# Optimization experiments

Measured on AMD Instinct MI355X. Metric: run time of the kernel, lower is better.

The kernel has to match this reference:

```python
import jax, jax.numpy as jnp
import numpy as np

B, S, D, H, M = 4, 1024, 1024, 16, 128
HD = D // H  # 64


def setup_inputs() -> dict:
    key = jax.random.key(0)
    ks = jax.random.split(key, 12)
    s = 0.02
    return {
        "x": jax.random.normal(ks[0], (B, S, D), dtype=jnp.float32),
        "Wq": jax.random.normal(ks[1], (D, D), dtype=jnp.float32) * s,
        "bq": jnp.zeros((D,), dtype=jnp.float32),
        "Wk": jax.random.normal(ks[2], (D, D), dtype=jnp.float32) * s,
        "bk": jnp.zeros((D,), dtype=jnp.float32),
        "Wv": jax.random.normal(ks[3], (D, D), dtype=jnp.float32) * s,
        "bv": jnp.zeros((D,), dtype=jnp.float32),
        "Wo": jax.random.normal(ks[4], (D, D), dtype=jnp.float32) * s,
        "bo": jnp.zeros((D,), dtype=jnp.float32),
        "u": jax.random.normal(ks[5], (H, HD), dtype=jnp.float32) * s,
        "v": jax.random.normal(ks[6], (H, HD), dtype=jnp.float32) * s,
    }


def _rel_sinusoid_emb():
    # [2M+1, HD] sinusoidal embeddings over relative offsets -M..M
    rel_range = jnp.arange(-M, M + 1, dtype=jnp.float32)
    inv_freq = 1.0 / (10000.0 ** (jnp.arange(0, HD, 2, dtype=jnp.float32) / HD))
    sinusoid = rel_range[:, None] * inv_freq[None, :]  # [2M+1, HD/2]
    emb = jnp.zeros((2 * M + 1, HD), dtype=jnp.float32)
    emb = emb.at[:, 0::2].set(jnp.sin(sinusoid))
    emb = emb.at[:, 1::2].set(jnp.cos(sinusoid))
    return emb


def reference(x, Wq, bq, Wk, bk, Wv, bv, Wo, bo, u, v):
    scale = 1.0 / np.sqrt(HD).astype(np.float32)

    def heads(t):  # [B,S,D] -> [B,H,S,HD]
        return t.reshape(B, S, H, HD).transpose(0, 2, 1, 3)

    q = heads(x @ Wq + bq)
    k = heads(x @ Wk + bk)
    vv = heads(x @ Wv + bv)

    rel_emb = _rel_sinusoid_emb()  # [2M+1, HD]
    pos = jnp.arange(S)
    rel_index = jnp.clip(pos[None, :] - pos[:, None], -M, M) + M  # [S,S] int

    q_u = q + u[None, :, None, :]
    q_v = q + v[None, :, None, :]

    content = jnp.einsum("bhid,bhjd->bhij", q_u, k) * scale  # [B,H,S,S]
    # einsum('bhid,ijd->bhij', q_v, rel_emb[rel_index]) == gather of per-bucket scores
    rel_all = jnp.einsum("bhid,rd->bhir", q_v, rel_emb) * scale  # [B,H,S,2M+1]
    rel_scores = jnp.take_along_axis(rel_all, rel_index[None, None, :, :], axis=-1)

    attn = jax.nn.softmax(content + rel_scores, axis=-1)
    out = jnp.einsum("bhij,bhjd->bhid", attn, vv)  # [B,H,S,HD]
    out = out.transpose(0, 2, 1, 3).reshape(B, S, D)
    return out @ Wo + bo
```

## Files before the change

### kernel.cpp

```cpp
#include <hip/hip_runtime.h>
#include <math.h>


#define BB 4
#define SS 1024
#define DD 1024
#define HH 16
#define HDIM 64
#define SCALE 0.125f
#define KMAX_BOUND 16.0f

typedef __attribute__((ext_vector_type(8))) short short8;
typedef __attribute__((ext_vector_type(4))) float f32x4;
typedef __attribute__((ext_vector_type(4))) unsigned short us4;
typedef unsigned short u16;

#define MFMA __builtin_amdgcn_mfma_f32_16x16x32_bf16

__device__ __forceinline__ float b2f(u16 v) {
  return __uint_as_float((unsigned)v << 16);
}
__device__ __forceinline__ u16 f2b(float f) {
  unsigned u = __float_as_uint(f);
  return (u16)((u + 0x7FFF + ((u >> 16) & 1)) >> 16);
}
__device__ __forceinline__ void gl_lds16(const u16* g, u16* l) {
  __builtin_amdgcn_global_load_lds(
      (const __attribute__((address_space(1))) unsigned int*)(g),
      (__attribute__((address_space(3))) unsigned int*)(l), 16, 0, 0);
}

__global__ __launch_bounds__(256) void prep(
    const float* __restrict__ x,
    const float* __restrict__ W0, const float* __restrict__ W1,
    const float* __restrict__ W2, const float* __restrict__ W3,
    u16* __restrict__ xb,
    u16* __restrict__ T0, u16* __restrict__ T1,
    u16* __restrict__ T2, u16* __restrict__ T3,
    u16* __restrict__ Eb) {
  __shared__ float t[64 * 68];
  const int bid = blockIdx.x, tid = threadIdx.x;
  if (bid < 2048) {
    const size_t i = ((size_t)bid * 256 + tid) * 8;
    float4 a = *reinterpret_cast<const float4*>(&x[i]);
    float4 b = *reinterpret_cast<const float4*>(&x[i + 4]);
    short8 v;
    v[0] = (short)f2b(a.x); v[1] = (short)f2b(a.y);
    v[2] = (short)f2b(a.z); v[3] = (short)f2b(a.w);
    v[4] = (short)f2b(b.x); v[5] = (short)f2b(b.y);
    v[6] = (short)f2b(b.z); v[7] = (short)f2b(b.w);
    *reinterpret_cast<short8*>(&xb[i]) = v;
  } else if (bid < 3072) {
    const int wz = bid - 2048;
    const int z = wz >> 8;
    const float* W = z == 0 ? W0 : z == 1 ? W1 : z == 2 ? W2 : W3;
    u16* T = z == 0 ? T0 : z == 1 ? T1 : z == 2 ? T2 : T3;
    const int k0 = ((wz >> 4) & 15) * 64, n0 = (wz & 15) * 64;
#pragma unroll
    for (int rd = 0; rd < 4; ++rd) {
      const int idx = rd * 256 + tid;
      const int r = idx >> 4, c4 = (idx & 15) * 4;
      *reinterpret_cast<float4*>(&t[r * 68 + c4]) =
          *reinterpret_cast<const float4*>(&W[(size_t)(k0 + r) * DD + n0 + c4]);
    }
    __syncthreads();
#pragma unroll
    for (int rd = 0; rd < 2; ++rd) {
      const int idx = rd * 256 + tid;
      const int rr = idx >> 3, cc = (idx & 7) * 8;
      short8 v;
#pragma unroll
      for (int e = 0; e < 8; ++e) v[e] = (short)f2b(t[(cc + e) * 68 + rr]);
      *reinterpret_cast<short8*>(&T[(size_t)(n0 + rr) * DD + k0 + cc]) = v;
    }
  } else {
    const int j = (bid - 3072) * 4 + (tid >> 6);
    const int d = tid & 63;
    const int pair = d >> 1;
    const float inv_freq =
        exp2f(-((float)(2 * pair) / 64.0f) * 13.287712379549449f);
    const float arg = (float)j * inv_freq;
    const float val = (d & 1) ? cosf(arg) : sinf(arg);
    Eb[j * 64 + d] = f2b(val);
  }
}

__global__ __launch_bounds__(256, 3) void gemm_mfma(
    const u16* __restrict__ A,
    const u16* __restrict__ W0, const u16* __restrict__ W1, const u16* __restrict__ W2,
    const float* __restrict__ b0, const float* __restrict__ b1, const float* __restrict__ b2,
    void* o0, void* o1, void* o2, int final_mode) {
  const int z = blockIdx.z;
  const u16* Bt = z == 0 ? W0 : z == 1 ? W1 : W2;
  const float* bias = z == 0 ? b0 : z == 1 ? b1 : b2;
  __shared__ u16 As0[128 * 32];
  __shared__ u16 Bs0[128 * 32];
  __shared__ u16 As1[128 * 32];
  __shared__ u16 Bs1[128 * 32];
  const int tid = threadIdx.x;
  const int bm = blockIdx.y * 128, bn = blockIdx.x * 128;
  const int lane = tid & 63, w = tid >> 6;
  const int wr = w >> 1, wc = w & 1;
  const int lr = lane & 15, lg = lane >> 4;

  const int r_i0 = 32 * w + (lane >> 2);
  const int r_i1 = r_i0 + 16;
  const int q0 = (lane & 3) ^ ((r_i0 >> 1) & 3);
  const int q1 = (lane & 3) ^ ((r_i1 >> 1) & 3);
  const u16* gA0 = &A[(size_t)(bm + r_i0) * DD + q0 * 8];
  const u16* gA1 = &A[(size_t)(bm + r_i1) * DD + q1 * 8];
  const u16* gB0 = &Bt[(size_t)(bn + r_i0) * DD + q0 * 8];
  const u16* gB1 = &Bt[(size_t)(bn + r_i1) * DD + q1 * 8];
  const int lo0 = (32 * w) * 32;
  const int lo1 = (32 * w + 16) * 32;

  const f32x4 Z4 = {0.f, 0.f, 0.f, 0.f};
  f32x4 acc[4][4];
#pragma unroll
  for (int m = 0; m < 4; ++m)
#pragma unroll
    for (int n = 0; n < 4; ++n) acc[m][n] = Z4;

  auto STAGE = [&](u16* Ab, u16* Bb, int kk) {
    gl_lds16(gA0 + kk, Ab + lo0);
    gl_lds16(gA1 + kk, Ab + lo1);
    gl_lds16(gB0 + kk, Bb + lo0);
    gl_lds16(gB1 + kk, Bb + lo1);
  };
  auto COMPUTE = [&](u16* Ab, u16* Bb) {
    short8 af[4], bf[4];
#pragma unroll
    for (int m = 0; m < 4; ++m) {
      const int row = wr * 64 + m * 16 + lr;
      af[m] = *reinterpret_cast<short8*>(&Ab[row * 32 + ((lg ^ ((row >> 1) & 3)) * 8)]);
    }
#pragma unroll
    for (int n = 0; n < 4; ++n) {
      const int row = wc * 64 + n * 16 + lr;
      bf[n] = *reinterpret_cast<short8*>(&Bb[row * 32 + ((lg ^ ((row >> 1) & 3)) * 8)]);
    }
#pragma unroll
    for (int m = 0; m < 4; ++m)
#pragma unroll
      for (int n = 0; n < 4; ++n)
        acc[m][n] = MFMA(af[m], bf[n], acc[m][n], 0, 0, 0);
  };

  STAGE(As0, Bs0, 0);
  __syncthreads();
  for (int k0 = 0; k0 < DD; k0 += 64) {
    STAGE(As1, Bs1, k0 + 32);
    COMPUTE(As0, Bs0);
    __syncthreads();
    if (k0 + 64 < DD) STAGE(As0, Bs0, k0 + 64);
    COMPUTE(As1, Bs1);
    __syncthreads();
  }

  const int mode = final_mode ? 2 : (z == 2 ? 1 : 0);
  u16* ob = (u16*)(z == 0 ? o0 : z == 1 ? o1 : o2);
  float* of = (float*)o0;
#pragma unroll
  for (int m = 0; m < 4; ++m) {
#pragma unroll
    for (int n = 0; n < 4; ++n) {
      const int col = bn + wc * 64 + n * 16 + lr;
      const float bv = bias[col];
      const int row0 = bm + wr * 64 + m * 16 + lg * 4;
      if (mode == 0) {
#pragma unroll
        for (int g = 0; g < 4; ++g)
          ob[(size_t)(row0 + g) * DD + col] = f2b(acc[m][n][g] + bv);
      } else if (mode == 2) {
#pragma unroll
        for (int g = 0; g < 4; ++g)
          of[(size_t)(row0 + g) * DD + col] = acc[m][n][g] + bv;
      } else {
        const int bI = row0 >> 10, s0 = row0 & 1023;
        us4 pk;
#pragma unroll
        for (int g = 0; g < 4; ++g) pk[g] = f2b(acc[m][n][g] + bv);
        *reinterpret_cast<us4*>(&ob[(size_t)col * 4096 + bI * 1024 + s0]) = pk;
      }
    }
  }
}

__global__ __launch_bounds__(256, 3) void attn_mfma(
    const u16* __restrict__ Qg, const u16* __restrict__ Kg,
    const u16* __restrict__ Vtg, const u16* __restrict__ Eb,
    const float* __restrict__ ub, const float* __restrict__ vb,
    u16* __restrict__ AO) {
  __shared__ u16 kk_l[64 * 128];
  __shared__ u16 vt_l[64 * 64];
  __shared__ u16 ps_l[128 * 64];
  __shared__ float ls_l[128];

  const int tid = threadIdx.x;
  const int it = blockIdx.x, h = blockIdx.y, b = blockIdx.z;
  const int i0 = it * 128;
  const int lane = tid & 63, w = tid >> 6;
  const int lr = lane & 15, lg = lane >> 4;
  const f32x4 Z4 = {0.f, 0.f, 0.f, 0.f};

  short8 aq[2][4];
  float Mrow[2], cL[2], cR[2];
#pragma unroll
  for (int m = 0; m < 2; ++m) {
    const int qpos = i0 + w * 32 + m * 16 + lr;
    const size_t qbase = (size_t)(b * SS + qpos) * DD + h * 64;
    const int iL = qpos >= 128 ? qpos - 128 : 0;
    const int iR = qpos <= 895 ? qpos + 128 : 1023;
    float nqu = 0.f, nqv = 0.f, clp = 0.f, crp = 0.f;
#pragma unroll
    for (int ks2 = 0; ks2 < 2; ++ks2) {
      const int d8 = ks2 * 32 + lg * 8;
      short8 q8 = *reinterpret_cast<const short8*>(&Qg[qbase + d8]);
      short8 e8 = *reinterpret_cast<const short8*>(&Eb[qpos * 64 + d8]);
      short8 eL8 = *reinterpret_cast<const short8*>(&Eb[iL * 64 + d8]);
      short8 eR8 = *reinterpret_cast<const short8*>(&Eb[iR * 64 + d8]);
      float us[8], vs[8];
      {
        float4 a = *reinterpret_cast<const float4*>(&ub[h * 64 + d8]);
        float4 d = *reinterpret_cast<const float4*>(&ub[h * 64 + d8 + 4]);
        us[0] = a.x; us[1] = a.y; us[2] = a.z; us[3] = a.w;
        us[4] = d.x; us[5] = d.y; us[6] = d.z; us[7] = d.w;
        float4 e = *reinterpret_cast<const float4*>(&vb[h * 64 + d8]);
        float4 f = *reinterpret_cast<const float4*>(&vb[h * 64 + d8 + 4]);
        vs[0] = e.x; vs[1] = e.y; vs[2] = e.z; vs[3] = e.w;
        vs[4] = f.x; vs[5] = f.y; vs[6] = f.z; vs[7] = f.w;
      }
      short8 xu, xr;
#pragma unroll
      for (int e = 0; e < 8; ++e) {
        const float qf = b2f((u16)q8[e]);
        xu[e] = (short)f2b(qf + us[e]);
        const float quf = b2f((u16)xu[e]);
        nqu = fmaf(quf, quf, nqu);
      }
#pragma unroll
      for (int p = 0; p < 4; ++p) {
        const float qv0 = b2f((u16)q8[2 * p]) + vs[2 * p];
        const float qv1 = b2f((u16)q8[2 * p + 1]) + vs[2 * p + 1];
        const float si = b2f((u16)e8[2 * p]), co = b2f((u16)e8[2 * p + 1]);
        const float r0 = qv0 * co + qv1 * si;
        const float r1 = qv1 * co - qv0 * si;
        xr[2 * p] = (short)f2b(r0);
        xr[2 * p + 1] = (short)f2b(r1);
        const float a0 = b2f((u16)xr[2 * p]), a1 = b2f((u16)xr[2 * p + 1]);
        nqv = fmaf(a0, a0, fmaf(a1, a1, nqv));
        clp = fmaf(a0, b2f((u16)eL8[2 * p]), fmaf(a1, b2f((u16)eL8[2 * p + 1]), clp));
        crp = fmaf(a0, b2f((u16)eR8[2 * p]), fmaf(a1, b2f((u16)eR8[2 * p + 1]), crp));
      }
      aq[m][ks2] = xu;
      aq[m][ks2 + 2] = xr;
    }
    nqu += __shfl_xor(nqu, 16); nqu += __shfl_xor(nqu, 32);
    nqv += __shfl_xor(nqv, 16); nqv += __shfl_xor(nqv, 32);
    clp += __shfl_xor(clp, 16); clp += __shfl_xor(clp, 32);
    crp += __shfl_xor(crp, 16); crp += __shfl_xor(crp, 32);
    Mrow[m] = 0.125f * KMAX_BOUND * sqrtf(nqu) + 0.7125f * sqrtf(nqv) + 0.03f;
    cL[m] = 0.125f * clp;
    cR[m] = 0.125f * crp;
  }

  float lsum[2] = {0.f, 0.f};
  f32x4 o_acc[2][4];
#pragma unroll
  for (int nq = 0; nq < 2; ++nq)
#pragma unroll
    for (int df = 0; df < 4; ++df) o_acc[nq][df] = Z4;

  const int srow = tid >> 2, sc4 = tid & 3;
  const int vr = tid >> 3, vc = tid & 7;
  const size_t kcol = (size_t)h * 64 + sc4 * 16;

  short8 kA, kB, eA, eB, v0r, v1r;
  {
    const size_t kbase = (size_t)(b * SS + srow) * DD + kcol;
    kA = *reinterpret_cast<const short8*>(&Kg[kbase]);
    kB = *reinterpret_cast<const short8*>(&Kg[kbase + 8]);
    const size_t ebase = (size_t)srow * 64 + sc4 * 16;
    eA = *reinterpret_cast<const short8*>(&Eb[ebase]);
    eB = *reinterpret_cast<const short8*>(&Eb[ebase + 8]);
    v0r = *reinterpret_cast<const short8*>(
        &Vtg[(size_t)(h * 64 + vr) * 4096 + b * SS + vc * 8]);
    v1r = *reinterpret_cast<const short8*>(
        &Vtg[(size_t)(h * 64 + vr + 32) * 4096 + b * SS + vc * 8]);
  }

  for (int jt = 0; jt < 16; ++jt) {
    const int j0 = jt * 64;
    __syncthreads();
    {
      const int rs = srow & 15;
      *reinterpret_cast<short8*>(&kk_l[srow * 128 + (((sc4 * 2) ^ rs) * 8)]) = kA;
      *reinterpret_cast<short8*>(&kk_l[srow * 128 + (((sc4 * 2 + 1) ^ rs) * 8)]) = kB;
      *reinterpret_cast<short8*>(&kk_l[srow * 128 + (((8 + sc4 * 2) ^ rs) * 8)]) = eA;
      *reinterpret_cast<short8*>(&kk_l[srow * 128 + (((9 + sc4 * 2) ^ rs) * 8)]) = eB;
      *reinterpret_cast<short8*>(&vt_l[vr * 64 + ((vc ^ (vr & 7)) * 8)]) = v0r;
      *reinterpret_cast<short8*>(&vt_l[(vr + 32) * 64 + ((vc ^ ((vr + 32) & 7)) * 8)]) = v1r;
    }
    __syncthreads();

    if (jt < 15) {
      const int jn = j0 + 64;
      const size_t kbase = (size_t)(b * SS + jn + srow) * DD + kcol;
      kA = *reinterpret_cast<const short8*>(&Kg[kbase]);
      kB = *reinterpret_cast<const short8*>(&Kg[kbase + 8]);
      const size_t ebase = (size_t)(jn + srow) * 64 + sc4 * 16;
      eA = *reinterpret_cast<const short8*>(&Eb[ebase]);
      eB = *reinterpret_cast<const short8*>(&Eb[ebase + 8]);
      v0r = *reinterpret_cast<const short8*>(
          &Vtg[(size_t)(h * 64 + vr) * 4096 + b * SS + jn + vc * 8]);
      v1r = *reinterpret_cast<const short8*>(
          &Vtg[(size_t)(h * 64 + vr + 32) * 4096 + b * SS + jn + vc * 8]);
    }

    const int roW = j0 - i0 - w * 32;
    if (roW < -191 || roW > 159) {
      const float fb0 = (roW < 0 ? cL[0] : cR[0]) - Mrow[0];
      const float fb1 = (roW < 0 ? cL[1] : cR[1]) - Mrow[1];
#pragma unroll
      for (int nf = 0; nf < 4; ++nf) {
        const int krow = nf * 16 + lr;
        short8 kf0 = *reinterpret_cast<short8*>(
            &kk_l[krow * 128 + ((lg ^ lr) * 8)]);
        short8 kf1 = *reinterpret_cast<short8*>(
            &kk_l[krow * 128 + (((4 + lg) ^ lr) * 8)]);
#pragma unroll
        for (int nq = 0; nq < 2; ++nq) {
          f32x4 s = MFMA(kf0, aq[nq][0], Z4, 0, 0, 0);
          s = MFMA(kf1, aq[nq][1], s, 0, 0, 0);
          const float base = nq == 0 ? fb0 : fb1;
          us4 pk;
#pragma unroll
          for (int g = 0; g < 4; ++g) {
            const float p = __expf(fmaf(s[g], SCALE, base));
            lsum[nq] += p;
            pk[g] = f2b(p);
          }
          const int prow = w * 32 + nq * 16 + lr;
          *reinterpret_cast<us4*>(
              &ps_l[prow * 64 + (((nf * 2 + (lg >> 1)) ^ (prow & 7)) * 8) +
                    4 * (lg & 1)]) = pk;
        }
      }
    } else {
#pragma unroll
      for (int nf = 0; nf < 4; ++nf) {
        const int krow = nf * 16 + lr;
        short8 kf0 = *reinterpret_cast<short8*>(
            &kk_l[krow * 128 + ((lg ^ lr) * 8)]);
        short8 kf1 = *reinterpret_cast<short8*>(
            &kk_l[krow * 128 + (((4 + lg) ^ lr) * 8)]);
        short8 kf2 = *reinterpret_cast<short8*>(
            &kk_l[krow * 128 + (((8 + lg) ^ lr) * 8)]);
        short8 kf3 = *reinterpret_cast<short8*>(
            &kk_l[krow * 128 + (((12 + lg) ^ lr) * 8)]);
#pragma unroll
        for (int nq = 0; nq < 2; ++nq) {
          f32x4 c = MFMA(kf0, aq[nq][0], Z4, 0, 0, 0);
          c = MFMA(kf1, aq[nq][1], c, 0, 0, 0);
          f32x4 t = MFMA(kf2, aq[nq][2], c, 0, 0, 0);
          t = MFMA(kf3, aq[nq][3], t, 0, 0, 0);
          const int rob = roW + nf * 16 + lg * 4 - nq * 16 - lr;
          const float bI = -Mrow[nq];
          const float bL = cL[nq] - Mrow[nq];
          const float bR = cR[nq] - Mrow[nq];
          us4 pk;
#pragma unroll
          for (int g = 0; g < 4; ++g) {
            const int ro = rob + g;
            const bool inr = (ro >= -128) && (ro <= 128);
            const float sval = inr ? t[g] : c[g];
            const float base = inr ? bI : (ro < -128 ? bL : bR);
            const float p = __expf(fmaf(sval, SCALE, base));
            lsum[nq] += p;
            pk[g] = f2b(p);
          }
          const int prow = w * 32 + nq * 16 + lr;
          *reinterpret_cast<us4*>(
              &ps_l[prow * 64 + (((nf * 2 + (lg >> 1)) ^ (prow & 7)) * 8) +
                    4 * (lg & 1)]) = pk;
        }
      }
    }

#pragma unroll
    for (int ks = 0; ks < 2; ++ks) {
      short8 ap0, ap1;
      {
        const int r0q = w * 32 + lr;
        ap0 = *reinterpret_cast<short8*>(
            &ps_l[r0q * 64 + (((ks * 4 + lg) ^ (r0q & 7)) * 8)]);
        const int r1q = w * 32 + 16 + lr;
        ap1 = *reinterpret_cast<short8*>(
            &ps_l[r1q * 64 + (((ks * 4 + lg) ^ (r1q & 7)) * 8)]);
      }
#pragma unroll
      for (int df = 0; df < 4; ++df) {
        const int vrow = df * 16 + lr;
        short8 vf = *reinterpret_cast<short8*>(
            &vt_l[vrow * 64 + (((ks * 4 + lg) ^ (vrow & 7)) * 8)]);
        o_acc[0][df] = MFMA(ap0, vf, o_acc[0][df], 0, 0, 0);
        o_acc[1][df] = MFMA(ap1, vf, o_acc[1][df], 0, 0, 0);
      }
    }
  }

#pragma unroll
  for (int nq = 0; nq < 2; ++nq) {
    lsum[nq] += __shfl_xor(lsum[nq], 16);
    lsum[nq] += __shfl_xor(lsum[nq], 32);
    ls_l[w * 32 + nq * 16 + lr] = lsum[nq];
  }
#pragma unroll
  for (int nq = 0; nq < 2; ++nq) {
#pragma unroll
    for (int g = 0; g < 4; ++g) {
      const float inv = 1.0f / ls_l[w * 32 + nq * 16 + lg * 4 + g];
      const int row = b * SS + i0 + w * 32 + nq * 16 + lg * 4 + g;
#pragma unroll
      for (int df = 0; df < 4; ++df) {
        AO[(size_t)row * DD + h * 64 + df * 16 + lr] =
            f2b(o_acc[nq][df][g] * inv);
      }
    }
  }
}

extern "C" void kernel_launch(void* const* d_in, const int* in_sizes, int n_in,
                              void* d_out, int out_size, void* d_ws, size_t ws_size,
                              hipStream_t stream) {
  const float* x  = (const float*)d_in[0];
  const float* Wq = (const float*)d_in[1];
  const float* bq = (const float*)d_in[2];
  const float* Wk = (const float*)d_in[3];
  const float* bk = (const float*)d_in[4];
  const float* Wv = (const float*)d_in[5];
  const float* bv = (const float*)d_in[6];
  const float* Wo = (const float*)d_in[7];
  const float* bo = (const float*)d_in[8];
  const float* u  = (const float*)d_in[9];
  const float* v  = (const float*)d_in[10];
  float* out = (float*)d_out;

  char* p = (char*)d_ws;
  const size_t TOK = (size_t)4096 * 1024 * 2;
  const size_t WSZ = (size_t)1024 * 1024 * 2;
  u16* Eb   = (u16*)p; p += (size_t)1024 * 64 * 2;
  u16* xb   = (u16*)p; p += TOK;
  u16* Wqt  = (u16*)p; p += WSZ;
  u16* Wkt  = (u16*)p; p += WSZ;
  u16* Wvt  = (u16*)p; p += WSZ;
  u16* Wot  = (u16*)p; p += WSZ;
  u16* Qb   = (u16*)p; p += TOK;
  u16* Kb   = (u16*)p; p += TOK;
  u16* Vt   = (u16*)p; p += TOK;
  u16* AOb  = (u16*)p; p += TOK;

  prep<<<3328, 256, 0, stream>>>(x, Wq, Wk, Wv, Wo, xb, Wqt, Wkt, Wvt, Wot, Eb);

  gemm_mfma<<<dim3(8, 32, 3), 256, 0, stream>>>(
      xb, Wqt, Wkt, Wvt, bq, bk, bv, Qb, Kb, Vt, 0);

  attn_mfma<<<dim3(SS / 128, HH, BB), 256, 0, stream>>>(
      Qb, Kb, Vt, Eb, u, v, AOb);

  gemm_mfma<<<dim3(8, 32, 1), 256, 0, stream>>>(
      AOb, Wot, Wot, Wot, bo, bo, bo, out, out, out, 1);
}
```

Measured before the change: 109.4 us.

## Halve attention query tile to 64 rows and use exp2 with folded log2e

The attention kernel now handles 64 query rows per block (16 per wave) instead of 128. This doubles the grid to 1024 blocks and shrinks registers and shared memory, with launch bounds raised to 4 blocks per SM. The log2e factor is folded into the scale and the bias terms so the softmax uses exp2f. The cost is that each K/V tile is loaded from global memory twice as often per query row, and there is less MFMA work per K/V fetch.

```diff
diff --git a/kernel.cpp b/kernel.cpp
--- a/kernel.cpp
+++ b/kernel.cpp
@@ -8,6 +8,8 @@
 #define HH 16
 #define HDIM 64
 #define SCALE 0.125f
+#define LOG2E 1.4426950408889634f
+#define SC2 (0.125f * LOG2E)
 #define KMAX_BOUND 16.0f
 
 typedef __attribute__((ext_vector_type(8))) short short8;
@@ -186,28 +188,27 @@
   }
 }
 
-__global__ __launch_bounds__(256, 3) void attn_mfma(
+__global__ __launch_bounds__(256, 4) void attn_mfma(
     const u16* __restrict__ Qg, const u16* __restrict__ Kg,
     const u16* __restrict__ Vtg, const u16* __restrict__ Eb,
     const float* __restrict__ ub, const float* __restrict__ vb,
     u16* __restrict__ AO) {
   __shared__ u16 kk_l[64 * 128];
   __shared__ u16 vt_l[64 * 64];
-  __shared__ u16 ps_l[128 * 64];
-  __shared__ float ls_l[128];
+  __shared__ u16 ps_l[64 * 64];
+  __shared__ float ls_l[64];
 
   const int tid = threadIdx.x;
   const int it = blockIdx.x, h = blockIdx.y, b = blockIdx.z;
-  const int i0 = it * 128;
+  const int i0 = it * 64;
   const int lane = tid & 63, w = tid >> 6;
   const int lr = lane & 15, lg = lane >> 4;
   const f32x4 Z4 = {0.f, 0.f, 0.f, 0.f};
 
-  short8 aq[2][4];
-  float Mrow[2], cL[2], cR[2];
-#pragma unroll
-  for (int m = 0; m < 2; ++m) {
-    const int qpos = i0 + w * 32 + m * 16 + lr;
+  short8 aq[4];
+  float bI2, bL2, bR2;
+  {
+    const int qpos = i0 + w * 16 + lr;
     const size_t qbase = (size_t)(b * SS + qpos) * DD + h * 64;
     const int iL = qpos >= 128 ? qpos - 128 : 0;
     const int iR = qpos <= 895 ? qpos + 128 : 1023;
@@ -252,24 +253,24 @@
         clp = fmaf(a0, b2f((u16)eL8[2 * p]), fmaf(a1, b2f((u16)eL8[2 * p + 1]), clp));
         crp = fmaf(a0, b2f((u16)eR8[2 * p]), fmaf(a1, b2f((u16)eR8[2 * p + 1]), crp));
       }
-      aq[m][ks2] = xu;
-      aq[m][ks2 + 2] = xr;
+      aq[ks2] = xu;
+      aq[ks2 + 2] = xr;
     }
     nqu += __shfl_xor(nqu, 16); nqu += __shfl_xor(nqu, 32);
     nqv += __shfl_xor(nqv, 16); nqv += __shfl_xor(nqv, 32);
     clp += __shfl_xor(clp, 16); clp += __shfl_xor(clp, 32);
     crp += __shfl_xor(crp, 16); crp += __shfl_xor(crp, 32);
-    Mrow[m] = 0.125f * KMAX_BOUND * sqrtf(nqu) + 0.7125f * sqrtf(nqv) + 0.03f;
-    cL[m] = 0.125f * clp;
-    cR[m] = 0.125f * crp;
-  }
-
-  float lsum[2] = {0.f, 0.f};
-  f32x4 o_acc[2][4];
-#pragma unroll
-  for (int nq = 0; nq < 2; ++nq)
-#pragma unroll
-    for (int df = 0; df < 4; ++df) o_acc[nq][df] = Z4;
+    const float Mrow =
+        0.125f * KMAX_BOUND * sqrtf(nqu) + 0.7125f * sqrtf(nqv) + 0.03f;
+    bI2 = -Mrow * LOG2E;
+    bL2 = (0.125f * clp - Mrow) * LOG2E;
+    bR2 = (0.125f * crp - Mrow) * LOG2E;
+  }
+
+  float lsum = 0.f;
+  f32x4 o_acc[4];
+#pragma unroll
+  for (int df = 0; df < 4; ++df) o_acc[df] = Z4;
 
   const int srow = tid >> 2, sc4 = tid & 3;
   const int vr = tid >> 3, vc = tid & 7;
@@ -317,10 +318,11 @@
           &Vtg[(size_t)(h * 64 + vr + 32) * 4096 + b * SS + jn + vc * 8]);
     }
 
-    const int roW = j0 - i0 - w * 32;
-    if (roW < -191 || roW > 159) {
-      const float fb0 = (roW < 0 ? cL[0] : cR[0]) - Mrow[0];
-      const float fb1 = (roW < 0 ? cL[1] : cR[1]) - Mrow[1];
+    const int roW = j0 - i0 - w * 16;
+    const int prow = w * 16 + lr;
+    const int psw = prow & 7;
+    if (roW < -191 || roW > 143) {
+      const float fb = (roW < 0 ? bL2 : bR2);
 #pragma unroll
       for (int nf = 0; nf < 4; ++nf) {
         const int krow = nf * 16 + lr;
@@ -328,23 +330,18 @@
             &kk_l[krow * 128 + ((lg ^ lr) * 8)]);
         short8 kf1 = *reinterpret_cast<short8*>(
             &kk_l[krow * 128 + (((4 + lg) ^ lr) * 8)]);
-#pragma unroll
-        for (int nq = 0; nq < 2; ++nq) {
-          f32x4 s = MFMA(kf0, aq[nq][0], Z4, 0, 0, 0);
-          s = MFMA(kf1, aq[nq][1], s, 0, 0, 0);
-          const float base = nq == 0 ? fb0 : fb1;
-          us4 pk;
-#pragma unroll
-          for (int g = 0; g < 4; ++g) {
-            const float p = __expf(fmaf(s[g], SCALE, base));
-            lsum[nq] += p;
-            pk[g] = f2b(p);
-          }
-          const int prow = w * 32 + nq * 16 + lr;
-          *reinterpret_cast<us4*>(
-              &ps_l[prow * 64 + (((nf * 2 + (lg >> 1)) ^ (prow & 7)) * 8) +
-                    4 * (lg & 1)]) = pk;
+        f32x4 s = MFMA(kf0, aq[0], Z4, 0, 0, 0);
+        s = MFMA(kf1, aq[1], s, 0, 0, 0);
+        us4 pk;
+#pragma unroll
+        for (int g = 0; g < 4; ++g) {
+          const float p = exp2f(fmaf(s[g], SC2, fb));
+          lsum += p;
+          pk[g] = f2b(p);
         }
+        *reinterpret_cast<us4*>(
+            &ps_l[prow * 64 + (((nf * 2 + (lg >> 1)) ^ psw) * 8) +
+                  4 * (lg & 1)]) = pk;
       }
     } else {
 #pragma unroll
@@ -358,74 +355,53 @@
             &kk_l[krow * 128 + (((8 + lg) ^ lr) * 8)]);
         short8 kf3 = *reinterpret_cast<short8*>(
             &kk_l[krow * 128 + (((12 + lg) ^ lr) * 8)]);
-#pragma unroll
-        for (int nq = 0; nq < 2; ++nq) {
-          f32x4 c = MFMA(kf0, aq[nq][0], Z4, 0, 0, 0);
-          c = MFMA(kf1, aq[nq][1], c, 0, 0, 0);
-          f32x4 t = MFMA(kf2, aq[nq][2], c, 0, 0, 0);
-          t = MFMA(kf3, aq[nq][3], t, 0, 0, 0);
-          const int rob = roW + nf * 16 + lg * 4 - nq * 16 - lr;
-          const float bI = -Mrow[nq];
-          const float bL = cL[nq] - Mrow[nq];
-          const float bR = cR[nq] - Mrow[nq];
-          us4 pk;
-#pragma unroll
-          for (int g = 0; g < 4; ++g) {
-            const int ro = rob + g;
-            const bool inr = (ro >= -128) && (ro <= 128);
-            const float sval = inr ? t[g] : c[g];
-            const float base = inr ? bI : (ro < -128 ? bL : bR);
-            const float p = __expf(fmaf(sval, SCALE, base));
-            lsum[nq] += p;
-            pk[g] = f2b(p);
-          }
-          const int prow = w * 32 + nq * 16 + lr;
-          *reinterpret_cast<us4*>(
-              &ps_l[prow * 64 + (((nf * 2 + (lg >> 1)) ^ (prow & 7)) * 8) +
-                    4 * (lg & 1)]) = pk;
+        f32x4 c = MFMA(kf0, aq[0], Z4, 0, 0, 0);
+        c = MFMA(kf1, aq[1], c, 0, 0, 0);
+        f32x4 t = MFMA(kf2, aq[2], c, 0, 0, 0);
+        t = MFMA(kf3, aq[3], t, 0, 0, 0);
+        const int rob = roW + nf * 16 + lg * 4 - lr;
+        us4 pk;
+#pragma unroll
+        for (int g = 0; g < 4; ++g) {
+          const int ro = rob + g;
+          const bool inr = (ro >= -128) && (ro <= 128);
+          const float sval = inr ? t[g] : c[g];
+          const float base = inr ? bI2 : (ro < -128 ? bL2 : bR2);
+          const float p = exp2f(fmaf(sval, SC2, base));
+          lsum += p;
+          pk[g] = f2b(p);
         }
+        *reinterpret_cast<us4*>(
+            &ps_l[prow * 64 + (((nf * 2 + (lg >> 1)) ^ psw) * 8) +
+                  4 * (lg & 1)]) = pk;
       }
     }
 
 #pragma unroll
     for (int ks = 0; ks < 2; ++ks) {
-      short8 ap0, ap1;
-      {
-        const int r0q = w * 32 + lr;
-        ap0 = *reinterpret_cast<short8*>(
-            &ps_l[r0q * 64 + (((ks * 4 + lg) ^ (r0q & 7)) * 8)]);
-        const int r1q = w * 32 + 16 + lr;
-        ap1 = *reinterpret_cast<short8*>(
-            &ps_l[r1q * 64 + (((ks * 4 + lg) ^ (r1q & 7)) * 8)]);
-      }
+      short8 ap = *reinterpret_cast<short8*>(
+          &ps_l[prow * 64 + (((ks * 4 + lg) ^ psw) * 8)]);
 #pragma unroll
       for (int df = 0; df < 4; ++df) {
         const int vrow = df * 16 + lr;
         short8 vf = *reinterpret_cast<short8*>(
             &vt_l[vrow * 64 + (((ks * 4 + lg) ^ (vrow & 7)) * 8)]);
-        o_acc[0][df] = MFMA(ap0, vf, o_acc[0][df], 0, 0, 0);
-        o_acc[1][df] = MFMA(ap1, vf, o_acc[1][df], 0, 0, 0);
-      }
-    }
-  }
-
-#pragma unroll
-  for (int nq = 0; nq < 2; ++nq) {
-    lsum[nq] += __shfl_xor(lsum[nq], 16);
-    lsum[nq] += __shfl_xor(lsum[nq], 32);
-    ls_l[w * 32 + nq * 16 + lr] = lsum[nq];
-  }
-#pragma unroll
-  for (int nq = 0; nq < 2; ++nq) {
-#pragma unroll
-    for (int g = 0; g < 4; ++g) {
-      const float inv = 1.0f / ls_l[w * 32 + nq * 16 + lg * 4 + g];
-      const int row = b * SS + i0 + w * 32 + nq * 16 + lg * 4 + g;
-#pragma unroll
-      for (int df = 0; df < 4; ++df) {
-        AO[(size_t)row * DD + h * 64 + df * 16 + lr] =
-            f2b(o_acc[nq][df][g] * inv);
-      }
+        o_acc[df] = MFMA(ap, vf, o_acc[df], 0, 0, 0);
+      }
+    }
+  }
+
+  lsum += __shfl_xor(lsum, 16);
+  lsum += __shfl_xor(lsum, 32);
+  ls_l[w * 16 + lr] = lsum;
+#pragma unroll
+  for (int g = 0; g < 4; ++g) {
+    const float inv = 1.0f / ls_l[w * 16 + lg * 4 + g];
+    const int row = b * SS + i0 + w * 16 + lg * 4 + g;
+#pragma unroll
+    for (int df = 0; df < 4; ++df) {
+      AO[(size_t)row * DD + h * 64 + df * 16 + lr] =
+          f2b(o_acc[df][g] * inv);
     }
   }
 }
@@ -465,7 +441,7 @@
   gemm_mfma<<<dim3(8, 32, 3), 256, 0, stream>>>(
       xb, Wqt, Wkt, Wvt, bq, bk, bv, Qb, Kb, Vt, 0);
 
-  attn_mfma<<<dim3(SS / 128, HH, BB), 256, 0, stream>>>(
+  attn_mfma<<<dim3(SS / 64, HH, BB), 256, 0, stream>>>(
       Qb, Kb, Vt, Eb, u, v, AOb);
 
   gemm_mfma<<<dim3(8, 32, 1), 256, 0, stream>>>(
```

Measured after the change: 114.9 us. 1.05x slower.

## Double-buffer K/E/V LDS tiles in attention to halve barriers per iteration

Applied to the files above, without the earlier changes.

The attention kernel now keeps two LDS buffers each for the K/E tile and the V tile. Each iteration stores the prefetched next tile into the alternate buffer after its PV MFMAs, so only one __syncthreads is needed per iteration instead of two. The per-row softmax bias terms are also precomputed once rather than rebuilt inside the loop. In exchange, LDS per block grows from about 40KB to about 64KB, and the launch bound drops from 3 to 2 blocks per CU, which lowers occupancy.

```diff
diff --git a/kernel.cpp b/kernel.cpp
--- a/kernel.cpp
+++ b/kernel.cpp
@@ -186,13 +186,15 @@
   }
 }
 
-__global__ __launch_bounds__(256, 3) void attn_mfma(
+__global__ __launch_bounds__(256, 2) void attn_mfma(
     const u16* __restrict__ Qg, const u16* __restrict__ Kg,
     const u16* __restrict__ Vtg, const u16* __restrict__ Eb,
     const float* __restrict__ ub, const float* __restrict__ vb,
     u16* __restrict__ AO) {
-  __shared__ u16 kk_l[64 * 128];
-  __shared__ u16 vt_l[64 * 64];
+  __shared__ u16 kk0[64 * 128];
+  __shared__ u16 kk1[64 * 128];
+  __shared__ u16 vt0[64 * 64];
+  __shared__ u16 vt1[64 * 64];
   __shared__ u16 ps_l[128 * 64];
   __shared__ float ls_l[128];
 
@@ -204,7 +206,7 @@
   const f32x4 Z4 = {0.f, 0.f, 0.f, 0.f};
 
   short8 aq[2][4];
-  float Mrow[2], cL[2], cR[2];
+  float bI[2], bL[2], bR[2];
 #pragma unroll
   for (int m = 0; m < 2; ++m) {
     const int qpos = i0 + w * 32 + m * 16 + lr;
@@ -259,9 +261,11 @@
     nqv += __shfl_xor(nqv, 16); nqv += __shfl_xor(nqv, 32);
     clp += __shfl_xor(clp, 16); clp += __shfl_xor(clp, 32);
     crp += __shfl_xor(crp, 16); crp += __shfl_xor(crp, 32);
-    Mrow[m] = 0.125f * KMAX_BOUND * sqrtf(nqu) + 0.7125f * sqrtf(nqv) + 0.03f;
-    cL[m] = 0.125f * clp;
-    cR[m] = 0.125f * crp;
+    const float Mrow =
+        0.125f * KMAX_BOUND * sqrtf(nqu) + 0.7125f * sqrtf(nqv) + 0.03f;
+    bI[m] = -Mrow;
+    bL[m] = 0.125f * clp - Mrow;
+    bR[m] = 0.125f * crp - Mrow;
   }
 
   float lsum[2] = {0.f, 0.f};
@@ -273,6 +277,7 @@
 
   const int srow = tid >> 2, sc4 = tid & 3;
   const int vr = tid >> 3, vc = tid & 7;
+  const int rs = srow & 15;
   const size_t kcol = (size_t)h * 64 + sc4 * 16;
 
   short8 kA, kB, eA, eB, v0r, v1r;
@@ -287,21 +292,21 @@
         &Vtg[(size_t)(h * 64 + vr) * 4096 + b * SS + vc * 8]);
     v1r = *reinterpret_cast<const short8*>(
         &Vtg[(size_t)(h * 64 + vr + 32) * 4096 + b * SS + vc * 8]);
-  }
+    *reinterpret_cast<short8*>(&kk0[srow * 128 + (((sc4 * 2) ^ rs) * 8)]) = kA;
+    *reinterpret_cast<short8*>(&kk0[srow * 128 + (((sc4 * 2 + 1) ^ rs) * 8)]) = kB;
+    *reinterpret_cast<short8*>(&kk0[srow * 128 + (((8 + sc4 * 2) ^ rs) * 8)]) = eA;
+    *reinterpret_cast<short8*>(&kk0[srow * 128 + (((9 + sc4 * 2) ^ rs) * 8)]) = eB;
+    *reinterpret_cast<short8*>(&vt0[vr * 64 + ((vc ^ (vr & 7)) * 8)]) = v0r;
+    *reinterpret_cast<short8*>(&vt0[(vr + 32) * 64 + ((vc ^ ((vr + 32) & 7)) * 8)]) = v1r;
+  }
+  __syncthreads();
 
   for (int jt = 0; jt < 16; ++jt) {
     const int j0 = jt * 64;
-    __syncthreads();
-    {
-      const int rs = srow & 15;
-      *reinterpret_cast<short8*>(&kk_l[srow * 128 + (((sc4 * 2) ^ rs) * 8)]) = kA;
-      *reinterpret_cast<short8*>(&kk_l[srow * 128 + (((sc4 * 2 + 1) ^ rs) * 8)]) = kB;
-      *reinterpret_cast<short8*>(&kk_l[srow * 128 + (((8 + sc4 * 2) ^ rs) * 8)]) = eA;
-      *reinterpret_cast<short8*>(&kk_l[srow * 128 + (((9 + sc4 * 2) ^ rs) * 8)]) = eB;
-      *reinterpret_cast<short8*>(&vt_l[vr * 64 + ((vc ^ (vr & 7)) * 8)]) = v0r;
-      *reinterpret_cast<short8*>(&vt_l[(vr + 32) * 64 + ((vc ^ ((vr + 32) & 7)) * 8)]) = v1r;
-    }
-    __syncthreads();
+    u16* kk_l = (jt & 1) ? kk1 : kk0;
+    u16* vt_l = (jt & 1) ? vt1 : vt0;
+    u16* kk_n = (jt & 1) ? kk0 : kk1;
+    u16* vt_n = (jt & 1) ? vt0 : vt1;
 
     if (jt < 15) {
       const int jn = j0 + 64;
@@ -319,8 +324,8 @@
 
     const int roW = j0 - i0 - w * 32;
     if (roW < -191 || roW > 159) {
-      const float fb0 = (roW < 0 ? cL[0] : cR[0]) - Mrow[0];
-      const float fb1 = (roW < 0 ? cL[1] : cR[1]) - Mrow[1];
+      const float fb0 = roW < 0 ? bL[0] : bR[0];
+      const float fb1 = roW < 0 ? bL[1] : bR[1];
 #pragma unroll
       for (int nf = 0; nf < 4; ++nf) {
         const int krow = nf * 16 + lr;
@@ -365,16 +370,13 @@
           f32x4 t = MFMA(kf2, aq[nq][2], c, 0, 0, 0);
           t = MFMA(kf3, aq[nq][3], t, 0, 0, 0);
           const int rob = roW + nf * 16 + lg * 4 - nq * 16 - lr;
-          const float bI = -Mrow[nq];
-          const float bL = cL[nq] - Mrow[nq];
-          const float bR = cR[nq] - Mrow[nq];
           us4 pk;
 #pragma unroll
           for (int g = 0; g < 4; ++g) {
             const int ro = rob + g;
             const bool inr = (ro >= -128) && (ro <= 128);
             const float sval = inr ? t[g] : c[g];
-            const float base = inr ? bI : (ro < -128 ? bL : bR);
+            const float base = inr ? bI[nq] : (ro < -128 ? bL[nq] : bR[nq]);
             const float p = __expf(fmaf(sval, SCALE, base));
             lsum[nq] += p;
             pk[g] = f2b(p);
@@ -407,6 +409,16 @@
         o_acc[1][df] = MFMA(ap1, vf, o_acc[1][df], 0, 0, 0);
       }
     }
+
+    if (jt < 15) {
+      *reinterpret_cast<short8*>(&kk_n[srow * 128 + (((sc4 * 2) ^ rs) * 8)]) = kA;
+      *reinterpret_cast<short8*>(&kk_n[srow * 128 + (((sc4 * 2 + 1) ^ rs) * 8)]) = kB;
+      *reinterpret_cast<short8*>(&kk_n[srow * 128 + (((8 + sc4 * 2) ^ rs) * 8)]) = eA;
+      *reinterpret_cast<short8*>(&kk_n[srow * 128 + (((9 + sc4 * 2) ^ rs) * 8)]) = eB;
+      *reinterpret_cast<short8*>(&vt_n[vr * 64 + ((vc ^ (vr & 7)) * 8)]) = v0r;
+      *reinterpret_cast<short8*>(&vt_n[(vr + 32) * 64 + ((vc ^ ((vr + 32) & 7)) * 8)]) = v1r;
+      __syncthreads();
+    }
   }
 
 #pragma unroll
@@ -415,6 +427,7 @@
     lsum[nq] += __shfl_xor(lsum[nq], 32);
     ls_l[w * 32 + nq * 16 + lr] = lsum[nq];
   }
+  __syncthreads();
 #pragma unroll
   for (int nq = 0; nq < 2; ++nq) {
 #pragma unroll
```

Result: no change. 108.7 us (-0.6%).
